# Performance work log

Hardware: AMD Instinct MI355X
Metric: run time of the kernel (lower is better)

## Reference

```python
import jax, jax.numpy as jnp
import numpy as np

B, S, D = 2, 2048, 1024
H = 16
DK = D // H
SCALE = 1.0 / np.sqrt(DK)

def setup_inputs() -> dict:
    key = jax.random.key(0)
    ks = jax.random.split(key, 11)
    std = 1.0 / np.sqrt(D)
    return {
        "query": jax.random.normal(ks[0], (B, S, D), jnp.float32),
        "key":   jax.random.normal(ks[1], (B, S, D), jnp.float32),
        "value": jax.random.normal(ks[2], (B, S, D), jnp.float32),
        "Wq": jax.random.normal(ks[3], (D, H * DK), jnp.float32) * std,
        "bq": jnp.zeros((H * DK,), jnp.float32),
        "Wk": jax.random.normal(ks[4], (D, H * DK), jnp.float32) * std,
        "bk": jnp.zeros((H * DK,), jnp.float32),
        "Wv": jax.random.normal(ks[5], (D, H * DK), jnp.float32) * std,
        "bv": jnp.zeros((H * DK,), jnp.float32),
        "Wo": jax.random.normal(ks[6], (D, D), jnp.float32) * std,
        "bo": jnp.zeros((D,), jnp.float32),
    }

def reference(query, key, value, Wq, bq, Wk, bk, Wv, bv, Wo, bo):
    b, s, _ = query.shape
    # projections -> [b, s, h, d_k]
    q = (query @ Wq + bq).reshape(b, s, H, DK)
    k = (key   @ Wk + bk).reshape(b, s, H, DK)
    v = (value @ Wv + bv).reshape(b, s, H, DK)
    # scores [b, i, j, h]
    scores = jnp.einsum('bihd,bjhd->bijh', q, k) * SCALE
    attn = jax.nn.softmax(scores, axis=2)  # softmax over key dim j
    # dropout rate 0.0 (eval mode) -> identity
    x = jnp.einsum('bijh,bjhd->bihd', attn, v).reshape(b, s, H * DK)
    return x @ Wo + bo
```

## Files before the change

### kernel.cpp

```cpp
#include <hip/hip_runtime.h>
#include <hip/hip_bf16.h>
#include <math.h>
#include <stdint.h>

constexpr int Bb = 2, Ss = 2048, Dd = 1024, Hh = 16;
constexpr int Mm = Bb * Ss;
constexpr int Nn = Dd;
constexpr int Kk = Dd;
constexpr float QSCALE = 0.125f * 1.44269504088896340736f;

typedef unsigned short ushort_t;
typedef __attribute__((ext_vector_type(8))) short bf16x8;
typedef __attribute__((ext_vector_type(4))) float f32x4;

__device__ __forceinline__ ushort_t f2bf(float f) {
  union { float f; unsigned u; } v; v.f = f;
  return (ushort_t)((v.u + 0x7fff + ((v.u >> 16) & 1)) >> 16);
}

__device__ __forceinline__ void load16_lds(const void* g, void* l) {
  __builtin_amdgcn_global_load_lds(
      (const __attribute__((address_space(1))) void*)(uintptr_t)g,
      (__attribute__((address_space(3))) void*)(uint32_t)(uintptr_t)l, 16, 0, 0);
}

__global__ __launch_bounds__(256) void convert_qkv(
    const float* __restrict__ q, const float* __restrict__ k,
    const float* __restrict__ v, ushort_t* __restrict__ out) {
  const int z = blockIdx.z;
  const float* src = (z == 0) ? q : (z == 1) ? k : v;
  ushort_t* dst = out + (size_t)z * Mm * Kk;
  const size_t idx = ((size_t)blockIdx.x * 256 + threadIdx.x) * 4;
  const float4 val = *(const float4*)(src + idx);
  ushort4 o;
  o.x = f2bf(val.x); o.y = f2bf(val.y); o.z = f2bf(val.z); o.w = f2bf(val.w);
  *(ushort4*)(dst + idx) = o;
}

__global__ __launch_bounds__(256) void transpose_w(
    const float* __restrict__ Wq, const float* __restrict__ Wk,
    const float* __restrict__ Wv, const float* __restrict__ Wo,
    ushort_t* __restrict__ Wt) {
  const int z = blockIdx.z;
  const float* W = (z == 0) ? Wq : (z == 1) ? Wk : (z == 2) ? Wv : Wo;
  ushort_t* out = Wt + (size_t)z * Kk * Nn;
  __shared__ float t[64][65];
  const int tid = threadIdx.x;
  const int n0 = blockIdx.x * 64, k0 = blockIdx.y * 64;
  const int lr = tid >> 4, lc = (tid & 15) * 4;
#pragma unroll
  for (int i = 0; i < 4; i++) {
    const int r = lr + i * 16;
    const float4 v = *(const float4*)(W + (size_t)(k0 + r) * Nn + n0 + lc);
    t[r][lc] = v.x; t[r][lc + 1] = v.y; t[r][lc + 2] = v.z; t[r][lc + 3] = v.w;
  }
  __syncthreads();
  const int n = tid >> 2, kc = (tid & 3) * 16;
  ushort_t tmp[16];
#pragma unroll
  for (int j = 0; j < 16; j++) tmp[j] = f2bf(t[kc + j][n]);
  ushort_t* op = out + (size_t)(n0 + n) * Kk + k0 + kc;
  ((uint4*)op)[0] = ((uint4*)tmp)[0];
  ((uint4*)op)[1] = ((uint4*)tmp)[1];
}

__global__ __launch_bounds__(256) void transpose_v(
    const ushort_t* __restrict__ Vp, ushort_t* __restrict__ Vt) {
  __shared__ ushort_t t[64][68];
  const int tid = threadIdx.x;
  const int s0 = blockIdx.x * 64, h = blockIdx.y, b = blockIdx.z;
  const int lr = tid >> 4, lc = (tid & 15) * 4;
#pragma unroll
  for (int i = 0; i < 4; i++) {
    const int r = lr + i * 16;
    const ushort4 v =
        *(const ushort4*)(Vp + (size_t)(b * Ss + s0 + r) * Dd + h * 64 + lc);
    *(ushort4*)&t[r][lc] = v;
  }
  __syncthreads();
  const int d = tid >> 2, sc = (tid & 3) * 16;
  ushort_t tmp[16];
#pragma unroll
  for (int j = 0; j < 16; j++) tmp[j] = t[sc + j][d];
  ushort_t* op = Vt + ((size_t)b * Dd + h * 64 + d) * Ss + s0 + sc;
  ((uint4*)op)[0] = ((uint4*)tmp)[0];
  ((uint4*)op)[1] = ((uint4*)tmp)[1];
}

template <int BN, bool OUT_BF16>
__global__ __launch_bounds__(256) void gemm_mfma(
    const ushort_t* __restrict__ Abase, size_t a_stride,
    const ushort_t* __restrict__ Wbase, size_t w_stride,
    const float* __restrict__ bias0, const float* __restrict__ bias1,
    const float* __restrict__ bias2, void* __restrict__ Cbase, size_t c_stride,
    float scale_z0) {
  constexpr int BM = 128, BK = 32;
  constexpr int WM = (BN == 128) ? 64 : 32;
  constexpr int MT_ = WM / 16, NT_ = 4;
  __shared__ ushort_t As[BM * BK];
  __shared__ ushort_t Bs[BN * BK];
  const int tid = threadIdx.x, lane = tid & 63, wid = tid >> 6;
  const int z = blockIdx.z;
  const ushort_t* A = Abase + (size_t)z * a_stride;
  const ushort_t* Wt = Wbase + (size_t)z * w_stride;
  const float* bias = (z == 0) ? bias0 : (z == 1) ? bias1 : bias2;
  const float sc = (z == 0) ? scale_z0 : 1.0f;
  const int m0 = blockIdx.y * BM, n0 = blockIdx.x * BN;
  const int wm = (BN == 128) ? (wid >> 1) * 64 : wid * 32;
  const int wn = (BN == 128) ? (wid & 1) * 64 : 0;
  const int quad = lane >> 4, r16 = lane & 15;
  const int srow = lane >> 2;
  const int scol = (lane & 3) * 8;

  f32x4 acc[MT_][NT_];
#pragma unroll
  for (int m = 0; m < MT_; m++)
#pragma unroll
    for (int n = 0; n < NT_; n++) acc[m][n] = f32x4{0.f, 0.f, 0.f, 0.f};

  for (int k0 = 0; k0 < Kk; k0 += BK) {
    __syncthreads();
#pragma unroll
    for (int i = 0; i < BM / 64; i++) {
      const int I = wid * (BM / 64) + i;
      load16_lds(A + (size_t)(m0 + I * 16 + srow) * Kk + k0 + scol, As + I * 512);
    }
#pragma unroll
    for (int i = 0; i < BN / 64; i++) {
      const int I = wid * (BN / 64) + i;
      load16_lds(Wt + (size_t)(n0 + I * 16 + srow) * Kk + k0 + scol, Bs + I * 512);
    }
    __syncthreads();
    bf16x8 af[MT_], bfr[NT_];
#pragma unroll
    for (int m = 0; m < MT_; m++)
      af[m] = *(const bf16x8*)(As + (wm + m * 16 + r16) * BK + quad * 8);
#pragma unroll
    for (int n = 0; n < NT_; n++)
      bfr[n] = *(const bf16x8*)(Bs + (wn + n * 16 + r16) * BK + quad * 8);
#pragma unroll
    for (int m = 0; m < MT_; m++)
#pragma unroll
      for (int n = 0; n < NT_; n++)
        acc[m][n] =
            __builtin_amdgcn_mfma_f32_16x16x32_bf16(af[m], bfr[n], acc[m][n], 0, 0, 0);
  }

#pragma unroll
  for (int m = 0; m < MT_; m++) {
#pragma unroll
    for (int n = 0; n < NT_; n++) {
      const int gc = n0 + wn + n * 16 + r16;
      const float bv = bias[gc];
#pragma unroll
      for (int r = 0; r < 4; r++) {
        const int gr = m0 + wm + m * 16 + quad * 4 + r;
        const float v = (acc[m][n][r] + bv) * sc;
        if (OUT_BF16)
          ((ushort_t*)Cbase)[(size_t)z * c_stride + (size_t)gr * Nn + gc] = f2bf(v);
        else
          ((float*)Cbase)[(size_t)z * c_stride + (size_t)gr * Nn + gc] = v;
      }
    }
  }
}

__global__ __launch_bounds__(256) void flash_mfma(
    const ushort_t* __restrict__ Qp, const ushort_t* __restrict__ Kp,
    const ushort_t* __restrict__ Vt, ushort_t* __restrict__ Xp) {
  __shared__ ushort_t Ks[64 * 64];
  __shared__ ushort_t Vts[64 * 64];
  __shared__ ushort_t Ps[128 * 72];
  const int tid = threadIdx.x, lane = tid & 63, wid = tid >> 6;
  const int qt = blockIdx.x, h = blockIdx.y, b = blockIdx.z;
  const int quad = lane >> 4, r16 = lane & 15;
  const int row8 = lane >> 3;
  const int colsw = ((lane & 7) ^ (row8 & 7)) * 8;
  const int swz = (r16 & 7);

  const ushort_t* Qg = Qp + ((size_t)(b * Ss + qt * 128)) * Dd + h * 64;
  const ushort_t* Kg = Kp + ((size_t)b * Ss) * Dd + h * 64;
  const ushort_t* Vg = Vt + ((size_t)b * Dd + h * 64) * Ss;

  bf16x8 qf[2][2];
#pragma unroll
  for (int nn = 0; nn < 2; nn++)
#pragma unroll
    for (int ks = 0; ks < 2; ks++)
      qf[nn][ks] = *(const bf16x8*)(
          Qg + (size_t)(wid * 32 + nn * 16 + r16) * Dd + ks * 32 + quad * 8);

  f32x4 acc[4][2];
  float rs[2] = {0.f, 0.f};
#pragma unroll
  for (int mt = 0; mt < 4; mt++)
#pragma unroll
    for (int nn = 0; nn < 2; nn++) acc[mt][nn] = f32x4{0.f, 0.f, 0.f, 0.f};

  for (int kt = 0; kt < Ss / 64; kt++) {
    __syncthreads();
#pragma unroll
    for (int i = 0; i < 2; i++) {
      const int I = wid * 2 + i;
      load16_lds(Kg + (size_t)(kt * 64 + I * 8 + row8) * Dd + colsw, Ks + I * 512);
      load16_lds(Vg + (size_t)(I * 8 + row8) * Ss + kt * 64 + colsw, Vts + I * 512);
    }
    __syncthreads();

    f32x4 sacc[4][2];
#pragma unroll
    for (int mm = 0; mm < 4; mm++)
#pragma unroll
      for (int nn = 0; nn < 2; nn++) sacc[mm][nn] = f32x4{0.f, 0.f, 0.f, 0.f};
#pragma unroll
    for (int ks = 0; ks < 2; ks++) {
      bf16x8 kf[4];
#pragma unroll
      for (int mm = 0; mm < 4; mm++)
        kf[mm] = *(const bf16x8*)(
            Ks + (mm * 16 + r16) * 64 + (((ks * 4 + quad) ^ swz) * 8));
#pragma unroll
      for (int mm = 0; mm < 4; mm++)
#pragma unroll
        for (int nn = 0; nn < 2; nn++)
          sacc[mm][nn] = __builtin_amdgcn_mfma_f32_16x16x32_bf16(
              kf[mm], qf[nn][ks], sacc[mm][nn], 0, 0, 0);
    }

#pragma unroll
    for (int mm = 0; mm < 4; mm++) {
#pragma unroll
      for (int nn = 0; nn < 2; nn++) {
        float p0 = exp2f(sacc[mm][nn][0]), p1 = exp2f(sacc[mm][nn][1]);
        float p2 = exp2f(sacc[mm][nn][2]), p3 = exp2f(sacc[mm][nn][3]);
        rs[nn] += (p0 + p1) + (p2 + p3);
        union { __hip_bfloat162 h; unsigned u; } lo, hi;
        lo.h = __float22bfloat162_rn(make_float2(p0, p1));
        hi.h = __float22bfloat162_rn(make_float2(p2, p3));
        *(uint2*)(Ps + (wid * 32 + nn * 16 + r16) * 72 + mm * 16 + quad * 4) =
            make_uint2(lo.u, hi.u);
      }
    }

#pragma unroll
    for (int ks = 0; ks < 2; ks++) {
      bf16x8 vf[4], pf[2];
#pragma unroll
      for (int mt = 0; mt < 4; mt++)
        vf[mt] = *(const bf16x8*)(
            Vts + (mt * 16 + r16) * 64 + (((ks * 4 + quad) ^ swz) * 8));
#pragma unroll
      for (int nn = 0; nn < 2; nn++)
        pf[nn] = *(const bf16x8*)(
            Ps + (wid * 32 + nn * 16 + r16) * 72 + ks * 32 + quad * 8);
#pragma unroll
      for (int mt = 0; mt < 4; mt++)
#pragma unroll
        for (int nn = 0; nn < 2; nn++)
          acc[mt][nn] = __builtin_amdgcn_mfma_f32_16x16x32_bf16(
              vf[mt], pf[nn], acc[mt][nn], 0, 0, 0);
    }
  }

  float inv[2];
#pragma unroll
  for (int nn = 0; nn < 2; nn++) {
    float s = rs[nn];
    s += __shfl_xor(s, 16, 64);
    s += __shfl_xor(s, 32, 64);
    inv[nn] = 1.0f / s;
  }

#pragma unroll
  for (int mt = 0; mt < 4; mt++) {
#pragma unroll
    for (int nn = 0; nn < 2; nn++) {
      ushort4 o;
      o.x = f2bf(acc[mt][nn][0] * inv[nn]);
      o.y = f2bf(acc[mt][nn][1] * inv[nn]);
      o.z = f2bf(acc[mt][nn][2] * inv[nn]);
      o.w = f2bf(acc[mt][nn][3] * inv[nn]);
      *(ushort4*)(Xp +
                  (size_t)(b * Ss + qt * 128 + wid * 32 + nn * 16 + r16) * Dd +
                  h * 64 + mt * 16 + quad * 4) = o;
    }
  }
}

extern "C" void kernel_launch(void* const* d_in, const int* in_sizes, int n_in,
                              void* d_out, int out_size, void* d_ws,
                              size_t ws_size, hipStream_t stream) {
  const float* q  = (const float*)d_in[0];
  const float* k  = (const float*)d_in[1];
  const float* v  = (const float*)d_in[2];
  const float* Wq = (const float*)d_in[3];
  const float* bq = (const float*)d_in[4];
  const float* Wk = (const float*)d_in[5];
  const float* bk = (const float*)d_in[6];
  const float* Wv = (const float*)d_in[7];
  const float* bv = (const float*)d_in[8];
  const float* Wo = (const float*)d_in[9];
  const float* bo = (const float*)d_in[10];

  ushort_t* ws = (ushort_t*)d_ws;
  const size_t MD = (size_t)Mm * Kk;
  const size_t KN = (size_t)Kk * Nn;
  ushort_t* qkvb = ws;
  ushort_t* Wt   = ws + 3 * MD;
  ushort_t* QKVp = Wt + 4 * KN;
  ushort_t* Vtp  = QKVp + 3 * MD;
  ushort_t* Xp   = qkvb;

  convert_qkv<<<dim3(4096, 1, 3), 256, 0, stream>>>(q, k, v, qkvb);
  transpose_w<<<dim3(16, 16, 4), 256, 0, stream>>>(Wq, Wk, Wv, Wo, Wt);
  gemm_mfma<128, true><<<dim3(Nn / 128, Mm / 128, 3), 256, 0, stream>>>(
      qkvb, MD, Wt, KN, bq, bk, bv, QKVp, MD, QSCALE);
  transpose_v<<<dim3(Ss / 64, Hh, Bb), 256, 0, stream>>>(QKVp + 2 * MD, Vtp);
  flash_mfma<<<dim3(Ss / 128, Hh, Bb), 256, 0, stream>>>(QKVp, QKVp + MD, Vtp, Xp);
  gemm_mfma<64, false><<<dim3(Nn / 64, Mm / 128, 1), 256, 0, stream>>>(
      Xp, 0, Wt + 3 * KN, 0, bo, bo, bo, d_out, 0, 1.0f);
}
```

Baseline: 255.3 us.

## Fuse V transpose into QKV GEMM epilogue and halve flash query tile

The V projection GEMM now writes its output directly in transposed [b, d, s] layout, which removes the separate transpose_v kernel and its extra global round trip. The flash attention kernel drops from 128 to 64 query rows per block, so it launches twice as many blocks with fewer registers and half the P shared buffer. In exchange, K and V tiles are reloaded by twice as many blocks. exp2f is replaced with the hardware exp2 builtin when it is available. The transposed V store in the epilogue writes 4-element column chunks, which may coalesce poorly.

```diff
diff --git a/kernel.cpp b/kernel.cpp
--- a/kernel.cpp
+++ b/kernel.cpp
@@ -12,6 +12,12 @@
 typedef unsigned short ushort_t;
 typedef __attribute__((ext_vector_type(8))) short bf16x8;
 typedef __attribute__((ext_vector_type(4))) float f32x4;
+
+#if __has_builtin(__builtin_amdgcn_exp2f)
+#define EXP2F(x) __builtin_amdgcn_exp2f(x)
+#else
+#define EXP2F(x) exp2f(x)
+#endif
 
 __device__ __forceinline__ ushort_t f2bf(float f) {
   union { float f; unsigned u; } v; v.f = f;
@@ -64,36 +70,13 @@
   ((uint4*)op)[1] = ((uint4*)tmp)[1];
 }
 
-__global__ __launch_bounds__(256) void transpose_v(
-    const ushort_t* __restrict__ Vp, ushort_t* __restrict__ Vt) {
-  __shared__ ushort_t t[64][68];
-  const int tid = threadIdx.x;
-  const int s0 = blockIdx.x * 64, h = blockIdx.y, b = blockIdx.z;
-  const int lr = tid >> 4, lc = (tid & 15) * 4;
-#pragma unroll
-  for (int i = 0; i < 4; i++) {
-    const int r = lr + i * 16;
-    const ushort4 v =
-        *(const ushort4*)(Vp + (size_t)(b * Ss + s0 + r) * Dd + h * 64 + lc);
-    *(ushort4*)&t[r][lc] = v;
-  }
-  __syncthreads();
-  const int d = tid >> 2, sc = (tid & 3) * 16;
-  ushort_t tmp[16];
-#pragma unroll
-  for (int j = 0; j < 16; j++) tmp[j] = t[sc + j][d];
-  ushort_t* op = Vt + ((size_t)b * Dd + h * 64 + d) * Ss + s0 + sc;
-  ((uint4*)op)[0] = ((uint4*)tmp)[0];
-  ((uint4*)op)[1] = ((uint4*)tmp)[1];
-}
-
 template <int BN, bool OUT_BF16>
 __global__ __launch_bounds__(256) void gemm_mfma(
     const ushort_t* __restrict__ Abase, size_t a_stride,
     const ushort_t* __restrict__ Wbase, size_t w_stride,
     const float* __restrict__ bias0, const float* __restrict__ bias1,
     const float* __restrict__ bias2, void* __restrict__ Cbase, size_t c_stride,
-    float scale_z0) {
+    float scale_z0, ushort_t* __restrict__ vt_out) {
   constexpr int BM = 128, BK = 32;
   constexpr int WM = (BN == 128) ? 64 : 32;
   constexpr int MT_ = WM / 16, NT_ = 4;
@@ -146,6 +129,25 @@
             __builtin_amdgcn_mfma_f32_16x16x32_bf16(af[m], bfr[n], acc[m][n], 0, 0, 0);
   }
 
+  if (vt_out != nullptr && z == 2) {
+#pragma unroll
+    for (int m = 0; m < MT_; m++) {
+      const int gr0 = m0 + wm + m * 16 + quad * 4;
+      const int bb = gr0 >> 11, s = gr0 & 2047;
+#pragma unroll
+      for (int n = 0; n < NT_; n++) {
+        const int gc = n0 + wn + n * 16 + r16;
+        const float bv = bias[gc];
+        ushort4 o;
+        o.x = f2bf(acc[m][n][0] + bv);
+        o.y = f2bf(acc[m][n][1] + bv);
+        o.z = f2bf(acc[m][n][2] + bv);
+        o.w = f2bf(acc[m][n][3] + bv);
+        *(ushort4*)(vt_out + ((size_t)bb * Dd + gc) * Ss + s) = o;
+      }
+    }
+    return;
+  }
 #pragma unroll
   for (int m = 0; m < MT_; m++) {
 #pragma unroll
@@ -170,7 +172,7 @@
     const ushort_t* __restrict__ Vt, ushort_t* __restrict__ Xp) {
   __shared__ ushort_t Ks[64 * 64];
   __shared__ ushort_t Vts[64 * 64];
-  __shared__ ushort_t Ps[128 * 72];
+  __shared__ ushort_t Ps[64 * 72];
   const int tid = threadIdx.x, lane = tid & 63, wid = tid >> 6;
   const int qt = blockIdx.x, h = blockIdx.y, b = blockIdx.z;
   const int quad = lane >> 4, r16 = lane & 15;
@@ -178,24 +180,20 @@
   const int colsw = ((lane & 7) ^ (row8 & 7)) * 8;
   const int swz = (r16 & 7);
 
-  const ushort_t* Qg = Qp + ((size_t)(b * Ss + qt * 128)) * Dd + h * 64;
+  const int qrow = wid * 16 + r16;
+  const ushort_t* Qg = Qp + ((size_t)(b * Ss + qt * 64)) * Dd + h * 64;
   const ushort_t* Kg = Kp + ((size_t)b * Ss) * Dd + h * 64;
   const ushort_t* Vg = Vt + ((size_t)b * Dd + h * 64) * Ss;
 
-  bf16x8 qf[2][2];
-#pragma unroll
-  for (int nn = 0; nn < 2; nn++)
-#pragma unroll
-    for (int ks = 0; ks < 2; ks++)
-      qf[nn][ks] = *(const bf16x8*)(
-          Qg + (size_t)(wid * 32 + nn * 16 + r16) * Dd + ks * 32 + quad * 8);
-
-  f32x4 acc[4][2];
-  float rs[2] = {0.f, 0.f};
-#pragma unroll
-  for (int mt = 0; mt < 4; mt++)
-#pragma unroll
-    for (int nn = 0; nn < 2; nn++) acc[mt][nn] = f32x4{0.f, 0.f, 0.f, 0.f};
+  bf16x8 qf[2];
+#pragma unroll
+  for (int ks = 0; ks < 2; ks++)
+    qf[ks] = *(const bf16x8*)(Qg + (size_t)qrow * Dd + ks * 32 + quad * 8);
+
+  f32x4 acc[4];
+  float rs = 0.f;
+#pragma unroll
+  for (int mt = 0; mt < 4; mt++) acc[mt] = f32x4{0.f, 0.f, 0.f, 0.f};
 
   for (int kt = 0; kt < Ss / 64; kt++) {
     __syncthreads();
@@ -207,11 +205,9 @@
     }
     __syncthreads();
 
-    f32x4 sacc[4][2];
-#pragma unroll
-    for (int mm = 0; mm < 4; mm++)
-#pragma unroll
-      for (int nn = 0; nn < 2; nn++) sacc[mm][nn] = f32x4{0.f, 0.f, 0.f, 0.f};
+    f32x4 sacc[4];
+#pragma unroll
+    for (int mm = 0; mm < 4; mm++) sacc[mm] = f32x4{0.f, 0.f, 0.f, 0.f};
 #pragma unroll
     for (int ks = 0; ks < 2; ks++) {
       bf16x8 kf[4];
@@ -221,69 +217,49 @@
             Ks + (mm * 16 + r16) * 64 + (((ks * 4 + quad) ^ swz) * 8));
 #pragma unroll
       for (int mm = 0; mm < 4; mm++)
-#pragma unroll
-        for (int nn = 0; nn < 2; nn++)
-          sacc[mm][nn] = __builtin_amdgcn_mfma_f32_16x16x32_bf16(
-              kf[mm], qf[nn][ks], sacc[mm][nn], 0, 0, 0);
+        sacc[mm] = __builtin_amdgcn_mfma_f32_16x16x32_bf16(
+            kf[mm], qf[ks], sacc[mm], 0, 0, 0);
     }
 
 #pragma unroll
     for (int mm = 0; mm < 4; mm++) {
-#pragma unroll
-      for (int nn = 0; nn < 2; nn++) {
-        float p0 = exp2f(sacc[mm][nn][0]), p1 = exp2f(sacc[mm][nn][1]);
-        float p2 = exp2f(sacc[mm][nn][2]), p3 = exp2f(sacc[mm][nn][3]);
-        rs[nn] += (p0 + p1) + (p2 + p3);
-        union { __hip_bfloat162 h; unsigned u; } lo, hi;
-        lo.h = __float22bfloat162_rn(make_float2(p0, p1));
-        hi.h = __float22bfloat162_rn(make_float2(p2, p3));
-        *(uint2*)(Ps + (wid * 32 + nn * 16 + r16) * 72 + mm * 16 + quad * 4) =
-            make_uint2(lo.u, hi.u);
-      }
+      float p0 = EXP2F(sacc[mm][0]), p1 = EXP2F(sacc[mm][1]);
+      float p2 = EXP2F(sacc[mm][2]), p3 = EXP2F(sacc[mm][3]);
+      rs += (p0 + p1) + (p2 + p3);
+      union { __hip_bfloat162 h; unsigned u; } lo, hi;
+      lo.h = __float22bfloat162_rn(make_float2(p0, p1));
+      hi.h = __float22bfloat162_rn(make_float2(p2, p3));
+      *(uint2*)(Ps + qrow * 72 + mm * 16 + quad * 4) = make_uint2(lo.u, hi.u);
     }
 
 #pragma unroll
     for (int ks = 0; ks < 2; ks++) {
-      bf16x8 vf[4], pf[2];
+      bf16x8 vf[4];
 #pragma unroll
       for (int mt = 0; mt < 4; mt++)
         vf[mt] = *(const bf16x8*)(
             Vts + (mt * 16 + r16) * 64 + (((ks * 4 + quad) ^ swz) * 8));
-#pragma unroll
-      for (int nn = 0; nn < 2; nn++)
-        pf[nn] = *(const bf16x8*)(
-            Ps + (wid * 32 + nn * 16 + r16) * 72 + ks * 32 + quad * 8);
+      const bf16x8 pf = *(const bf16x8*)(Ps + qrow * 72 + ks * 32 + quad * 8);
 #pragma unroll
       for (int mt = 0; mt < 4; mt++)
-#pragma unroll
-        for (int nn = 0; nn < 2; nn++)
-          acc[mt][nn] = __builtin_amdgcn_mfma_f32_16x16x32_bf16(
-              vf[mt], pf[nn], acc[mt][nn], 0, 0, 0);
-    }
-  }
-
-  float inv[2];
-#pragma unroll
-  for (int nn = 0; nn < 2; nn++) {
-    float s = rs[nn];
-    s += __shfl_xor(s, 16, 64);
-    s += __shfl_xor(s, 32, 64);
-    inv[nn] = 1.0f / s;
-  }
+        acc[mt] = __builtin_amdgcn_mfma_f32_16x16x32_bf16(
+            vf[mt], pf, acc[mt], 0, 0, 0);
+    }
+  }
+
+  rs += __shfl_xor(rs, 16, 64);
+  rs += __shfl_xor(rs, 32, 64);
+  const float inv = 1.0f / rs;
 
 #pragma unroll
   for (int mt = 0; mt < 4; mt++) {
-#pragma unroll
-    for (int nn = 0; nn < 2; nn++) {
-      ushort4 o;
-      o.x = f2bf(acc[mt][nn][0] * inv[nn]);
-      o.y = f2bf(acc[mt][nn][1] * inv[nn]);
-      o.z = f2bf(acc[mt][nn][2] * inv[nn]);
-      o.w = f2bf(acc[mt][nn][3] * inv[nn]);
-      *(ushort4*)(Xp +
-                  (size_t)(b * Ss + qt * 128 + wid * 32 + nn * 16 + r16) * Dd +
-                  h * 64 + mt * 16 + quad * 4) = o;
-    }
+    ushort4 o;
+    o.x = f2bf(acc[mt][0] * inv);
+    o.y = f2bf(acc[mt][1] * inv);
+    o.z = f2bf(acc[mt][2] * inv);
+    o.w = f2bf(acc[mt][3] * inv);
+    *(ushort4*)(Xp + (size_t)(b * Ss + qt * 64 + qrow) * Dd +
+                h * 64 + mt * 16 + quad * 4) = o;
   }
 }
 
@@ -314,9 +290,8 @@
   convert_qkv<<<dim3(4096, 1, 3), 256, 0, stream>>>(q, k, v, qkvb);
   transpose_w<<<dim3(16, 16, 4), 256, 0, stream>>>(Wq, Wk, Wv, Wo, Wt);
   gemm_mfma<128, true><<<dim3(Nn / 128, Mm / 128, 3), 256, 0, stream>>>(
-      qkvb, MD, Wt, KN, bq, bk, bv, QKVp, MD, QSCALE);
-  transpose_v<<<dim3(Ss / 64, Hh, Bb), 256, 0, stream>>>(QKVp + 2 * MD, Vtp);
-  flash_mfma<<<dim3(Ss / 128, Hh, Bb), 256, 0, stream>>>(QKVp, QKVp + MD, Vtp, Xp);
+      qkvb, MD, Wt, KN, bq, bk, bv, QKVp, MD, QSCALE, Vtp);
+  flash_mfma<<<dim3(Ss / 64, Hh, Bb), 256, 0, stream>>>(QKVp, QKVp + MD, Vtp, Xp);
   gemm_mfma<64, false><<<dim3(Nn / 64, Mm / 128, 1), 256, 0, stream>>>(
-      Xp, 0, Wt + 3 * KN, 0, bo, bo, bo, d_out, 0, 1.0f);
-}
+      Xp, 0, Wt + 3 * KN, 0, bo, bo, bo, d_out, 0, 1.0f, nullptr);
+}
```

Result: faster. 248.8 us (-2.6%).
